# Kernel optimization log

Measured on AMD Instinct MI355X. Metric: run time of the kernel, lower is better.

## Reference

```python
import jax, jax.numpy as jnp
import numpy as np

NA = 50000   # nodes of type 'a'
NB = 50000   # nodes of type 'b'
E = 800000   # edges per cross relation
D = 256      # input feature dim == hidden_dim (SAGEConv lazy in-dim)
H = 256      # hidden_dim
EMB = 128    # embedding_dim
L = 2        # num_layer
# relation order in stacked weights: 0=(a,to,b), 1=(b,to,a), 2=(a,self_loop,a), 3=(b,self_loop,b)


def setup_inputs() -> dict:
    key = jax.random.key(0)
    ks = jax.random.split(key, 8)
    x_a = jax.random.normal(ks[0], (NA, D), jnp.float32)
    x_b = jax.random.normal(ks[1], (NB, D), jnp.float32)
    edge_ab = jax.random.randint(ks[2], (2, E), 0, NA, dtype=jnp.int32)  # row0: src in a, row1: dst in b
    edge_ba = jax.random.randint(ks[3], (2, E), 0, NB, dtype=jnp.int32)  # row0: src in b, row1: dst in a
    s = 1.0 / np.sqrt(H)
    Wl = jax.random.normal(ks[4], (L, 4, H, H), jnp.float32) * s  # lin_l weight (on aggregated neighbors)
    bl = jnp.zeros((L, 4, H), jnp.float32)                         # lin_l bias
    Wr = jax.random.normal(ks[5], (L, 4, H, H), jnp.float32) * s  # lin_r weight (root/self), no bias
    lin_W = jax.random.normal(ks[6], (H, EMB), jnp.float32) * s
    lin_b = jnp.zeros((EMB,), jnp.float32)
    return dict(x_a=x_a, x_b=x_b, edge_ab=edge_ab, edge_ba=edge_ba,
                Wl=Wl, bl=bl, Wr=Wr, lin_W=lin_W, lin_b=lin_b)


def _sage(x_src, x_dst, src, dst, n_dst, Wl, bl, Wr):
    # SAGEConv: mean-aggregate neighbor features, then lin_l(agg) + lin_r(x_dst)
    agg = jax.ops.segment_sum(x_src[src], dst, num_segments=n_dst)           # [n_dst, H]
    cnt = jax.ops.segment_sum(jnp.ones(src.shape, x_src.dtype), dst, num_segments=n_dst)
    mean = agg / jnp.maximum(cnt, 1.0)[:, None]                               # isolated dst -> 0
    return mean @ Wl + bl + x_dst @ Wr


def _sage_self(x, Wl, bl, Wr):
    # self-loop relation: each node has exactly one neighbor (itself), mean == x
    return x @ Wl + bl + x @ Wr


def reference(x_a, x_b, edge_ab, edge_ba, Wl, bl, Wr, lin_W, lin_b):
    xa, xb = x_a, x_b
    for l in range(L):
        new_a = (_sage(xb, xa, edge_ba[0], edge_ba[1], xa.shape[0], Wl[l, 1], bl[l, 1], Wr[l, 1])
                 + _sage_self(xa, Wl[l, 2], bl[l, 2], Wr[l, 2]))
        new_b = (_sage(xa, xb, edge_ab[0], edge_ab[1], xb.shape[0], Wl[l, 0], bl[l, 0], Wr[l, 0])
                 + _sage_self(xb, Wl[l, 3], bl[l, 3], Wr[l, 3]))
        xa, xb = jax.nn.relu(new_a), jax.nn.relu(new_b)
    return xa @ lin_W + lin_b, xb @ lin_W + lin_b
```

## Files before the change

kernel.cpp:

```cpp
#include <hip/hip_runtime.h>
#include <hip/hip_bf16.h>

#define NNA 50000
#define NNB 50000
#define NE  800000
#define HD  256
#define EMBD 128

typedef __attribute__((ext_vector_type(4))) int            i32x4;
typedef __attribute__((ext_vector_type(4))) float          f32x4;
typedef __attribute__((ext_vector_type(8))) short          bf16x8;
typedef __attribute__((ext_vector_type(4))) unsigned short u16x4;
typedef __attribute__((ext_vector_type(8))) unsigned short u16x8;

static __device__ __forceinline__ float bf2f(unsigned short u) {
  union { unsigned int i; float f; } v; v.i = ((unsigned int)u) << 16; return v.f;
}
static __device__ __forceinline__ unsigned short f2bf(float f) {
  __hip_bfloat16 h = __float2bfloat16(f);
  return *reinterpret_cast<unsigned short*>(&h);
}

static __device__ __forceinline__ void gload_lds16(const void* g, void* l) {
  __builtin_amdgcn_global_load_lds((const __attribute__((address_space(1))) void*)g,
                                   (__attribute__((address_space(3))) void*)l, 16, 0, 0);
}

__global__ void k_prep(const float* __restrict__ Wl, const float* __restrict__ Wr,
                       const float* __restrict__ bl, const float* __restrict__ linW,
                       unsigned short* __restrict__ WcatT, float* __restrict__ bias,
                       unsigned short* __restrict__ linWT) {
  int id = blockIdx.x * 256 + threadIdx.x;
  if (id < 2 * 2 * 512 * 256) {
    int n = id & 255;
    int k = (id >> 8) & 511;
    int t = (id >> 17) & 1;
    int l = id >> 18;
    int rn = (t == 0) ? 1 : 0;
    int rs = (t == 0) ? 2 : 3;
    float v;
    if (k < HD) {
      v = Wl[((l * 4 + rn) * HD + k) * HD + n];
    } else {
      int kk = k - HD;
      v = Wr[((l * 4 + rn) * HD + kk) * HD + n]
        + Wl[((l * 4 + rs) * HD + kk) * HD + n]
        + Wr[((l * 4 + rs) * HD + kk) * HD + n];
    }
    WcatT[((l * 2 + t) * HD + n) * 512 + k] = f2bf(v);
    return;
  }
  int id1 = id - 2 * 2 * 512 * 256;
  if (id1 < 2 * 2 * 256) {
    int n = id1 & 255; int t = (id1 >> 8) & 1; int l = id1 >> 9;
    int rn = (t == 0) ? 1 : 0;
    int rs = (t == 0) ? 2 : 3;
    bias[id1] = bl[(l * 4 + rn) * HD + n] + bl[(l * 4 + rs) * HD + n];
    return;
  }
  int id2 = id1 - 2 * 2 * 256;
  if (id2 < EMBD * HD) {
    int k = id2 & 255; int n = id2 >> 8;
    linWT[n * HD + k] = f2bf(linW[k * EMBD + n]);
  }
}

__global__ void k_convert(const float* __restrict__ xa, const float* __restrict__ xb,
                          unsigned short* __restrict__ out) {
  const int n4a = NNA * HD / 4;
  const int n4  = (NNA + NNB) * HD / 4;
  int i = blockIdx.x * blockDim.x + threadIdx.x;
  int stride = gridDim.x * blockDim.x;
  for (; i < n4; i += stride) {
    const float* src = (i < n4a) ? (xa + (size_t)i * 4) : (xb + (size_t)(i - n4a) * 4);
    f32x4 v = *reinterpret_cast<const f32x4*>(src);
    u16x4 o;
    o[0] = f2bf(v[0]); o[1] = f2bf(v[1]); o[2] = f2bf(v[2]); o[3] = f2bf(v[3]);
    reinterpret_cast<u16x4*>(out)[i] = o;
  }
}

__global__ void k_fill(const int* __restrict__ e_ba, const int* __restrict__ e_ab,
                       int* __restrict__ cnt_a, int* __restrict__ slots_a,
                       int* __restrict__ cnt_b, int* __restrict__ slots_b) {
  int e = blockIdx.x * 256 + threadIdx.x;
  if (e < NE) {
    int src = e_ba[e];
    int dst = e_ba[NE + e];
    int pos = atomicAdd(&cnt_a[dst], 1);
    if (pos < 64) slots_a[dst * 64 + pos] = src;
  } else if (e < 2 * NE) {
    int f = e - NE;
    int src = e_ab[f];
    int dst = e_ab[NE + f];
    int pos = atomicAdd(&cnt_b[dst], 1);
    if (pos < 64) slots_b[dst * 64 + pos] = src;
  }
}

__global__ __launch_bounds__(256)
void k_aggregate(const unsigned short* __restrict__ xa,
                 const unsigned short* __restrict__ xb,
                 const int* __restrict__ slots_a, const int* __restrict__ cnt_a,
                 const int* __restrict__ slots_b, const int* __restrict__ cnt_b,
                 unsigned short* __restrict__ mean_a, unsigned short* __restrict__ mean_b) {
  int w = blockIdx.x * 4 + (threadIdx.x >> 6);
  int lane = threadIdx.x & 63;
  const unsigned short* xsrc;
  const int* sl;
  int deg;
  unsigned short* outp;
  if (w < NNA) {
    xsrc = xb; sl = slots_a + (size_t)w * 64; deg = cnt_a[w];
    outp = mean_a + (size_t)w * HD;
  } else {
    int v = w - NNA;
    xsrc = xa; sl = slots_b + (size_t)v * 64; deg = cnt_b[v];
    outp = mean_b + (size_t)v * HD;
  }
  int m = deg < 64 ? deg : 64;
  int s_all = sl[lane];
  const int half = lane >> 5;
  const int l31 = lane & 31;

  float acc[8];
#pragma unroll
  for (int k = 0; k < 8; ++k) acc[k] = 0.f;

  int j = 0;
  for (; j + 8 <= m; j += 8) {
    int sj[4];
#pragma unroll
    for (int i = 0; i < 4; ++i) sj[i] = __shfl(s_all, j + 2 * i + half);
    u16x8 v[4];
#pragma unroll
    for (int i = 0; i < 4; ++i)
      v[i] = *reinterpret_cast<const u16x8*>(xsrc + (size_t)sj[i] * HD + l31 * 8);
#pragma unroll
    for (int i = 0; i < 4; ++i)
#pragma unroll
      for (int k = 0; k < 8; ++k) acc[k] += bf2f(v[i][k]);
  }
  for (; j + 2 <= m; j += 2) {
    int sj = __shfl(s_all, j + half);
    u16x8 v = *reinterpret_cast<const u16x8*>(xsrc + (size_t)sj * HD + l31 * 8);
#pragma unroll
    for (int k = 0; k < 8; ++k) acc[k] += bf2f(v[k]);
  }
  if (j < m && half == 0) {
    int sj = __shfl(s_all, j);
    u16x8 v = *reinterpret_cast<const u16x8*>(xsrc + (size_t)sj * HD + l31 * 8);
#pragma unroll
    for (int k = 0; k < 8; ++k) acc[k] += bf2f(v[k]);
  }

#pragma unroll
  for (int k = 0; k < 8; ++k) acc[k] += __shfl_xor(acc[k], 32);

  float inv = deg > 0 ? 1.0f / (float)deg : 0.0f;
  if (half == 0) {
    u16x8 o;
#pragma unroll
    for (int k = 0; k < 8; ++k) o[k] = f2bf(acc[k] * inv);
    *reinterpret_cast<u16x8*>(outp + l31 * 8) = o;
  }
}

template <bool RELU, bool OUTF32>
__global__ __launch_bounds__(256)
void k_gemm(const unsigned short* __restrict__ Alo,
            const unsigned short* __restrict__ Ahi,
            const unsigned short* __restrict__ BT,
            const float* __restrict__ bias,
            void* __restrict__ Cout,
            int M, int N, int Ktot, int Klo,
            long long sA, long long sB, long long sBias, long long sCbytes) {
  const int z = blockIdx.z;
  Alo += (long long)z * sA;
  Ahi += (long long)z * sA;
  BT += (long long)z * sB;
  bias += (long long)z * sBias;
  Cout = (void*)((char*)Cout + (long long)z * sCbytes);

  __shared__ char smem[65536];
  const int t = threadIdx.x;
  const int bm = blockIdx.x, bn = blockIdx.y;
  const int lane = t & 63, wid = t >> 6;
  const int wm = wid >> 1, wn = wid & 1;
  const int l15 = lane & 15, l4 = lane >> 4;
  const int rgrp = lane >> 3;
  const int boff = (((lane & 7) ^ rgrp) << 4);

  f32x4 acc[4][4];
#pragma unroll
  for (int i = 0; i < 4; ++i)
#pragma unroll
    for (int j = 0; j < 4; ++j) acc[i][j] = (f32x4){0.f, 0.f, 0.f, 0.f};

  const int nks = Ktot >> 6;

  auto stage = [&](int ks, int buf) {
    const int kglob = ks << 6;
    const unsigned short* Asrc = (kglob < Klo) ? Alo : Ahi;
    const int kbase = (kglob < Klo) ? kglob : (kglob - Klo);
    char* sA_ = smem + buf * 16384;
    char* sB_ = smem + 32768 + buf * 16384;
#pragma unroll
    for (int i = 0; i < 4; ++i) {
      int rloc = wid * 32 + i * 8;
      int rA = bm * 128 + rloc + rgrp;
      if (rA >= M) rA = M - 1;
      const char* ga = (const char*)(Asrc + (size_t)rA * HD + kbase) + boff;
      gload_lds16(ga, sA_ + rloc * 128);
      int rB = bn * 128 + rloc + rgrp;
      const char* gb = (const char*)(BT + (size_t)rB * Ktot + kglob) + boff;
      gload_lds16(gb, sB_ + rloc * 128);
    }
  };

  stage(0, 0);
  __syncthreads();

  for (int ks = 0; ks < nks; ++ks) {
    if (ks + 1 < nks) stage(ks + 1, (ks + 1) & 1);
    const char* sA_ = smem + (ks & 1) * 16384;
    const char* sB_ = smem + 32768 + (ks & 1) * 16384;
#pragma unroll
    for (int kk = 0; kk < 2; ++kk) {
      bf16x8 af[4], bfr[4];
#pragma unroll
      for (int f = 0; f < 4; ++f) {
        int r = wm * 64 + f * 16 + l15;
        af[f] = *reinterpret_cast<const bf16x8*>(
            sA_ + r * 128 + ((kk * 64 + l4 * 16) ^ ((r & 7) << 4)));
        int n = wn * 64 + f * 16 + l15;
        bfr[f] = *reinterpret_cast<const bf16x8*>(
            sB_ + n * 128 + ((kk * 64 + l4 * 16) ^ ((n & 7) << 4)));
      }
#pragma unroll
      for (int fm = 0; fm < 4; ++fm)
#pragma unroll
        for (int fn = 0; fn < 4; ++fn)
          acc[fm][fn] = __builtin_amdgcn_mfma_f32_16x16x32_bf16(af[fm], bfr[fn], acc[fm][fn], 0, 0, 0);
    }
    __syncthreads();
  }

#pragma unroll
  for (int fm = 0; fm < 4; ++fm) {
    int row0 = bm * 128 + wm * 64 + fm * 16 + l4 * 4;
#pragma unroll
    for (int fn = 0; fn < 4; ++fn) {
      int col = bn * 128 + wn * 64 + fn * 16 + l15;
      float bv = bias[col];
      f32x4 d = acc[fm][fn];
#pragma unroll
      for (int r = 0; r < 4; ++r) {
        int rg = row0 + r;
        if (rg < M) {
          float v = d[r] + bv;
          if (RELU) v = v > 0.f ? v : 0.f;
          if (OUTF32)
            reinterpret_cast<float*>(Cout)[(size_t)rg * N + col] = v;
          else
            reinterpret_cast<unsigned short*>(Cout)[(size_t)rg * N + col] = f2bf(v);
        }
      }
    }
  }
}


extern "C" void kernel_launch(void* const* d_in, const int* in_sizes, int n_in,
                              void* d_out, int out_size, void* d_ws, size_t ws_size,
                              hipStream_t stream) {
  const float* x_a  = (const float*)d_in[0];
  const float* x_b  = (const float*)d_in[1];
  const int*   e_ab = (const int*)d_in[2];
  const int*   e_ba = (const int*)d_in[3];
  const float* Wl   = (const float*)d_in[4];
  const float* bl   = (const float*)d_in[5];
  const float* Wr   = (const float*)d_in[6];
  const float* linW = (const float*)d_in[7];
  const float* linb = (const float*)d_in[8];
  float* out = (float*)d_out;

  char* ws = (char*)d_ws;
  size_t off = 0;
  auto alloc = [&](size_t bytes) {
    char* p = ws + off;
    off += (bytes + 255) & ~(size_t)255;
    return p;
  };
  unsigned short* x0   = (unsigned short*)alloc((size_t)2 * NNA * HD * 2);
  unsigned short* x1   = (unsigned short*)alloc((size_t)2 * NNA * HD * 2);
  unsigned short* mean = (unsigned short*)alloc((size_t)2 * NNA * HD * 2);
  int* slots_a = (int*)alloc((size_t)NNA * 64 * 4);
  int* slots_b = (int*)alloc((size_t)NNB * 64 * 4);
  int* cnt_a   = (int*)alloc((size_t)NNA * 4);
  int* cnt_b   = (int*)alloc((size_t)NNB * 4);
  unsigned short* wcatT  = (unsigned short*)alloc((size_t)2 * 2 * 256 * 512 * 2);
  float*          biasv  = (float*)alloc((size_t)2 * 2 * 256 * 4);
  unsigned short* linWT  = (unsigned short*)alloc((size_t)EMBD * HD * 2);
  (void)ws_size; (void)in_sizes; (void)n_in; (void)out_size;

  hipMemsetAsync(cnt_a, 0, (size_t)NNA * 4, stream);
  hipMemsetAsync(cnt_b, 0, (size_t)NNB * 4, stream);

  k_prep<<<(2 * 2 * 512 * 256 + 1024 + 32768 + 255) / 256, 256, 0, stream>>>(
      Wl, Wr, bl, linW, wcatT, biasv, linWT);
  k_convert<<<2048, 256, 0, stream>>>(x_a, x_b, x0);
  k_fill<<<(2 * NE + 255) / 256, 256, 0, stream>>>(e_ba, e_ab, cnt_a, slots_a, cnt_b, slots_b);

  unsigned short* xcur = x0;
  unsigned short* xnxt = x1;

  for (int l = 0; l < 2; ++l) {
    k_aggregate<<<(NNA + NNB) / 4, 256, 0, stream>>>(
        xcur, xcur + (size_t)NNA * HD, slots_a, cnt_a, slots_b, cnt_b,
        mean, mean + (size_t)NNA * HD);
    dim3 g((NNA + 127) / 128, 2, 2);
    k_gemm<true, false><<<g, 256, 0, stream>>>(
        mean, xcur, wcatT + (size_t)l * 2 * 256 * 512, biasv + l * 2 * 256, xnxt,
        NNA, 256, 512, 256,
        (long long)NNA * HD, 256 * 512, 256, (long long)NNA * HD * 2);
    unsigned short* tmp = xcur; xcur = xnxt; xnxt = tmp;
  }

  dim3 gf((NNA + 127) / 128, 1, 2);
  k_gemm<false, true><<<gf, 256, 0, stream>>>(
      xcur, xcur, linWT, linb, out,
      NNA, EMBD, 256, 256,
      (long long)NNA * HD, 0, 0, (long long)NNA * EMBD * 4);
}
```

Baseline: 527.5 us.

## Build compact CSR adjacency with 16-bit indices and fuse front-end kernels

```diff
diff --git a/kernel.cpp b/kernel.cpp
--- a/kernel.cpp
+++ b/kernel.cpp
@@ -7,6 +7,11 @@
 #define HD  256
 #define EMBD 128
 
+#define CONV_BLOCKS 2048
+#define COUNT_BLOCKS ((2 * NE) / 256)
+#define PREP_IDS (2 * 2 * 512 * 256 + 1024 + 32768)
+#define PREP_BLOCKS ((PREP_IDS + 255) / 256)
+
 typedef __attribute__((ext_vector_type(4))) int            i32x4;
 typedef __attribute__((ext_vector_type(4))) float          f32x4;
 typedef __attribute__((ext_vector_type(8))) short          bf16x8;
@@ -26,100 +31,143 @@
                                    (__attribute__((address_space(3))) void*)l, 16, 0, 0);
 }
 
-__global__ void k_prep(const float* __restrict__ Wl, const float* __restrict__ Wr,
-                       const float* __restrict__ bl, const float* __restrict__ linW,
-                       unsigned short* __restrict__ WcatT, float* __restrict__ bias,
-                       unsigned short* __restrict__ linWT) {
+__global__ __launch_bounds__(256)
+void k_front(const float* __restrict__ xa, const float* __restrict__ xb,
+             unsigned short* __restrict__ xout,
+             const int* __restrict__ e_ba, const int* __restrict__ e_ab,
+             int* __restrict__ cnt_a, int* __restrict__ cnt_b,
+             const float* __restrict__ Wl, const float* __restrict__ Wr,
+             const float* __restrict__ bl, const float* __restrict__ linW,
+             unsigned short* __restrict__ WcatT, float* __restrict__ bias,
+             unsigned short* __restrict__ linWT) {
+  int b = blockIdx.x;
+  if (b < CONV_BLOCKS) {
+    const int n4a = NNA * HD / 4;
+    const int n4  = (NNA + NNB) * HD / 4;
+    int i = b * 256 + threadIdx.x;
+    const int stride = CONV_BLOCKS * 256;
+    for (; i < n4; i += stride) {
+      const float* src = (i < n4a) ? (xa + (size_t)i * 4) : (xb + (size_t)(i - n4a) * 4);
+      f32x4 v = *reinterpret_cast<const f32x4*>(src);
+      u16x4 o;
+      o[0] = f2bf(v[0]); o[1] = f2bf(v[1]); o[2] = f2bf(v[2]); o[3] = f2bf(v[3]);
+      reinterpret_cast<u16x4*>(xout)[i] = o;
+    }
+    return;
+  }
+  b -= CONV_BLOCKS;
+  if (b < COUNT_BLOCKS) {
+    int e = b * 256 + threadIdx.x;
+    if (e < NE) {
+      int dst = e_ba[NE + e];
+      atomicAdd(&cnt_a[dst], 1);
+    } else {
+      int f = e - NE;
+      int dst = e_ab[NE + f];
+      atomicAdd(&cnt_b[dst], 1);
+    }
+    return;
+  }
+  b -= COUNT_BLOCKS;
+  {
+    int id = b * 256 + threadIdx.x;
+    if (id < 2 * 2 * 512 * 256) {
+      int n = id & 255;
+      int k = (id >> 8) & 511;
+      int t = (id >> 17) & 1;
+      int l = id >> 18;
+      int rn = (t == 0) ? 1 : 0;
+      int rs = (t == 0) ? 2 : 3;
+      float v;
+      if (k < HD) {
+        v = Wl[((l * 4 + rn) * HD + k) * HD + n];
+      } else {
+        int kk = k - HD;
+        v = Wr[((l * 4 + rn) * HD + kk) * HD + n]
+          + Wl[((l * 4 + rs) * HD + kk) * HD + n]
+          + Wr[((l * 4 + rs) * HD + kk) * HD + n];
+      }
+      WcatT[((l * 2 + t) * HD + n) * 512 + k] = f2bf(v);
+      return;
+    }
+    int id1 = id - 2 * 2 * 512 * 256;
+    if (id1 < 2 * 2 * 256) {
+      int n = id1 & 255; int t = (id1 >> 8) & 1; int l = id1 >> 9;
+      int rn = (t == 0) ? 1 : 0;
+      int rs = (t == 0) ? 2 : 3;
+      bias[id1] = bl[(l * 4 + rn) * HD + n] + bl[(l * 4 + rs) * HD + n];
+      return;
+    }
+    int id2 = id1 - 2 * 2 * 256;
+    if (id2 < EMBD * HD) {
+      int k = id2 & 255; int n = id2 >> 8;
+      linWT[n * HD + k] = f2bf(linW[k * EMBD + n]);
+    }
+  }
+}
+
+__global__ __launch_bounds__(256)
+void k_offsets(const int* __restrict__ cnt_a, const int* __restrict__ cnt_b,
+               unsigned* __restrict__ offs, unsigned* __restrict__ pos,
+               unsigned* __restrict__ tail) {
   int id = blockIdx.x * 256 + threadIdx.x;
-  if (id < 2 * 2 * 512 * 256) {
-    int n = id & 255;
-    int k = (id >> 8) & 511;
-    int t = (id >> 17) & 1;
-    int l = id >> 18;
-    int rn = (t == 0) ? 1 : 0;
-    int rs = (t == 0) ? 2 : 3;
-    float v;
-    if (k < HD) {
-      v = Wl[((l * 4 + rn) * HD + k) * HD + n];
-    } else {
-      int kk = k - HD;
-      v = Wr[((l * 4 + rn) * HD + kk) * HD + n]
-        + Wl[((l * 4 + rs) * HD + kk) * HD + n]
-        + Wr[((l * 4 + rs) * HD + kk) * HD + n];
-    }
-    WcatT[((l * 2 + t) * HD + n) * 512 + k] = f2bf(v);
-    return;
-  }
-  int id1 = id - 2 * 2 * 512 * 256;
-  if (id1 < 2 * 2 * 256) {
-    int n = id1 & 255; int t = (id1 >> 8) & 1; int l = id1 >> 9;
-    int rn = (t == 0) ? 1 : 0;
-    int rs = (t == 0) ? 2 : 3;
-    bias[id1] = bl[(l * 4 + rn) * HD + n] + bl[(l * 4 + rs) * HD + n];
-    return;
-  }
-  int id2 = id1 - 2 * 2 * 256;
-  if (id2 < EMBD * HD) {
-    int k = id2 & 255; int n = id2 >> 8;
-    linWT[n * HD + k] = f2bf(linW[k * EMBD + n]);
-  }
-}
-
-__global__ void k_convert(const float* __restrict__ xa, const float* __restrict__ xb,
-                          unsigned short* __restrict__ out) {
-  const int n4a = NNA * HD / 4;
-  const int n4  = (NNA + NNB) * HD / 4;
-  int i = blockIdx.x * blockDim.x + threadIdx.x;
-  int stride = gridDim.x * blockDim.x;
-  for (; i < n4; i += stride) {
-    const float* src = (i < n4a) ? (xa + (size_t)i * 4) : (xb + (size_t)(i - n4a) * 4);
-    f32x4 v = *reinterpret_cast<const f32x4*>(src);
-    u16x4 o;
-    o[0] = f2bf(v[0]); o[1] = f2bf(v[1]); o[2] = f2bf(v[2]); o[3] = f2bf(v[3]);
-    reinterpret_cast<u16x4*>(out)[i] = o;
-  }
-}
-
-__global__ void k_fill(const int* __restrict__ e_ba, const int* __restrict__ e_ab,
-                       int* __restrict__ cnt_a, int* __restrict__ slots_a,
-                       int* __restrict__ cnt_b, int* __restrict__ slots_b) {
+  int lane = threadIdx.x & 63;
+  unsigned deg = 0;
+  if (id < NNA) deg = (unsigned)cnt_a[id];
+  else if (id < NNA + NNB) deg = (unsigned)cnt_b[id - NNA];
+  unsigned v = deg;
+#pragma unroll
+  for (int d = 1; d < 64; d <<= 1) {
+    unsigned n = __shfl_up(v, d);
+    if (lane >= d) v += n;
+  }
+  unsigned tot = __shfl(v, 63);
+  unsigned base = 0;
+  if (lane == 0) base = atomicAdd(tail, tot);
+  base = __shfl(base, 0);
+  unsigned o = base + v - deg;
+  if (id < NNA + NNB) { offs[id] = o; pos[id] = o; }
+}
+
+__global__ __launch_bounds__(256)
+void k_scatter(const int* __restrict__ e_ba, const int* __restrict__ e_ab,
+               unsigned* __restrict__ pos, unsigned short* __restrict__ csr) {
   int e = blockIdx.x * 256 + threadIdx.x;
   if (e < NE) {
     int src = e_ba[e];
     int dst = e_ba[NE + e];
-    int pos = atomicAdd(&cnt_a[dst], 1);
-    if (pos < 64) slots_a[dst * 64 + pos] = src;
+    unsigned p = atomicAdd(&pos[dst], 1u);
+    csr[p] = (unsigned short)src;
   } else if (e < 2 * NE) {
     int f = e - NE;
     int src = e_ab[f];
     int dst = e_ab[NE + f];
-    int pos = atomicAdd(&cnt_b[dst], 1);
-    if (pos < 64) slots_b[dst * 64 + pos] = src;
+    unsigned p = atomicAdd(&pos[NNA + dst], 1u);
+    csr[p] = (unsigned short)src;
   }
 }
 
 __global__ __launch_bounds__(256)
 void k_aggregate(const unsigned short* __restrict__ xa,
                  const unsigned short* __restrict__ xb,
-                 const int* __restrict__ slots_a, const int* __restrict__ cnt_a,
-                 const int* __restrict__ slots_b, const int* __restrict__ cnt_b,
+                 const unsigned* __restrict__ offs,
+                 const int* __restrict__ cnt_a, const int* __restrict__ cnt_b,
+                 const unsigned short* __restrict__ csr,
                  unsigned short* __restrict__ mean_a, unsigned short* __restrict__ mean_b) {
   int w = blockIdx.x * 4 + (threadIdx.x >> 6);
   int lane = threadIdx.x & 63;
   const unsigned short* xsrc;
-  const int* sl;
   int deg;
   unsigned short* outp;
+  unsigned off0 = offs[w];
   if (w < NNA) {
-    xsrc = xb; sl = slots_a + (size_t)w * 64; deg = cnt_a[w];
+    xsrc = xb; deg = cnt_a[w];
     outp = mean_a + (size_t)w * HD;
   } else {
     int v = w - NNA;
-    xsrc = xa; sl = slots_b + (size_t)v * 64; deg = cnt_b[v];
+    xsrc = xa; deg = cnt_b[v];
     outp = mean_b + (size_t)v * HD;
   }
-  int m = deg < 64 ? deg : 64;
-  int s_all = sl[lane];
   const int half = lane >> 5;
   const int l31 = lane & 31;
 
@@ -127,31 +175,38 @@
 #pragma unroll
   for (int k = 0; k < 8; ++k) acc[k] = 0.f;
 
-  int j = 0;
-  for (; j + 8 <= m; j += 8) {
-    int sj[4];
-#pragma unroll
-    for (int i = 0; i < 4; ++i) sj[i] = __shfl(s_all, j + 2 * i + half);
-    u16x8 v[4];
-#pragma unroll
-    for (int i = 0; i < 4; ++i)
-      v[i] = *reinterpret_cast<const u16x8*>(xsrc + (size_t)sj[i] * HD + l31 * 8);
-#pragma unroll
-    for (int i = 0; i < 4; ++i)
-#pragma unroll
-      for (int k = 0; k < 8; ++k) acc[k] += bf2f(v[i][k]);
-  }
-  for (; j + 2 <= m; j += 2) {
-    int sj = __shfl(s_all, j + half);
-    u16x8 v = *reinterpret_cast<const u16x8*>(xsrc + (size_t)sj * HD + l31 * 8);
-#pragma unroll
-    for (int k = 0; k < 8; ++k) acc[k] += bf2f(v[k]);
-  }
-  if (j < m && half == 0) {
-    int sj = __shfl(s_all, j);
-    u16x8 v = *reinterpret_cast<const u16x8*>(xsrc + (size_t)sj * HD + l31 * 8);
-#pragma unroll
-    for (int k = 0; k < 8; ++k) acc[k] += bf2f(v[k]);
+  for (int j0 = 0; j0 < deg; j0 += 64) {
+    int mm = deg - j0;
+    if (mm > 64) mm = 64;
+    int s_all = 0;
+    if (j0 + lane < deg) s_all = (int)csr[off0 + j0 + lane];
+
+    int j = 0;
+    for (; j + 8 <= mm; j += 8) {
+      int sj[4];
+#pragma unroll
+      for (int i = 0; i < 4; ++i) sj[i] = __shfl(s_all, j + 2 * i + half);
+      u16x8 v[4];
+#pragma unroll
+      for (int i = 0; i < 4; ++i)
+        v[i] = *reinterpret_cast<const u16x8*>(xsrc + (size_t)sj[i] * HD + l31 * 8);
+#pragma unroll
+      for (int i = 0; i < 4; ++i)
+#pragma unroll
+        for (int k = 0; k < 8; ++k) acc[k] += bf2f(v[i][k]);
+    }
+    for (; j + 2 <= mm; j += 2) {
+      int sj = __shfl(s_all, j + half);
+      u16x8 v = *reinterpret_cast<const u16x8*>(xsrc + (size_t)sj * HD + l31 * 8);
+#pragma unroll
+      for (int k = 0; k < 8; ++k) acc[k] += bf2f(v[k]);
+    }
+    if (j < mm && half == 0) {
+      int sj = __shfl(s_all, j);
+      u16x8 v = *reinterpret_cast<const u16x8*>(xsrc + (size_t)sj * HD + l31 * 8);
+#pragma unroll
+      for (int k = 0; k < 8; ++k) acc[k] += bf2f(v[k]);
+    }
   }
 
 #pragma unroll
@@ -295,29 +350,30 @@
   unsigned short* x0   = (unsigned short*)alloc((size_t)2 * NNA * HD * 2);
   unsigned short* x1   = (unsigned short*)alloc((size_t)2 * NNA * HD * 2);
   unsigned short* mean = (unsigned short*)alloc((size_t)2 * NNA * HD * 2);
-  int* slots_a = (int*)alloc((size_t)NNA * 64 * 4);
-  int* slots_b = (int*)alloc((size_t)NNB * 64 * 4);
-  int* cnt_a   = (int*)alloc((size_t)NNA * 4);
-  int* cnt_b   = (int*)alloc((size_t)NNB * 4);
+  int*      cnt_a = (int*)alloc((size_t)(NNA + NNB + 64) * 4);
+  int*      cnt_b = cnt_a + NNA;
+  unsigned* tail  = (unsigned*)(cnt_a + NNA + NNB);
+  unsigned* offs  = (unsigned*)alloc((size_t)(NNA + NNB) * 4);
+  unsigned* pos   = (unsigned*)alloc((size_t)(NNA + NNB) * 4);
+  unsigned short* csr = (unsigned short*)alloc((size_t)(2 * NE + 64) * 2);
   unsigned short* wcatT  = (unsigned short*)alloc((size_t)2 * 2 * 256 * 512 * 2);
   float*          biasv  = (float*)alloc((size_t)2 * 2 * 256 * 4);
   unsigned short* linWT  = (unsigned short*)alloc((size_t)EMBD * HD * 2);
   (void)ws_size; (void)in_sizes; (void)n_in; (void)out_size;
 
-  hipMemsetAsync(cnt_a, 0, (size_t)NNA * 4, stream);
-  hipMemsetAsync(cnt_b, 0, (size_t)NNB * 4, stream);
-
-  k_prep<<<(2 * 2 * 512 * 256 + 1024 + 32768 + 255) / 256, 256, 0, stream>>>(
-      Wl, Wr, bl, linW, wcatT, biasv, linWT);
-  k_convert<<<2048, 256, 0, stream>>>(x_a, x_b, x0);
-  k_fill<<<(2 * NE + 255) / 256, 256, 0, stream>>>(e_ba, e_ab, cnt_a, slots_a, cnt_b, slots_b);
+  hipMemsetAsync(cnt_a, 0, (size_t)(NNA + NNB + 64) * 4, stream);
+
+  k_front<<<CONV_BLOCKS + COUNT_BLOCKS + PREP_BLOCKS, 256, 0, stream>>>(
+      x_a, x_b, x0, e_ba, e_ab, cnt_a, cnt_b, Wl, Wr, bl, linW, wcatT, biasv, linWT);
+  k_offsets<<<(NNA + NNB + 255) / 256, 256, 0, stream>>>(cnt_a, cnt_b, offs, pos, tail);
+  k_scatter<<<(2 * NE + 255) / 256, 256, 0, stream>>>(e_ba, e_ab, pos, csr);
 
   unsigned short* xcur = x0;
   unsigned short* xnxt = x1;
 
   for (int l = 0; l < 2; ++l) {
     k_aggregate<<<(NNA + NNB) / 4, 256, 0, stream>>>(
-        xcur, xcur + (size_t)NNA * HD, slots_a, cnt_a, slots_b, cnt_b,
+        xcur, xcur + (size_t)NNA * HD, offs, cnt_a, cnt_b, csr,
         mean, mean + (size_t)NNA * HD);
     dim3 g((NNA + 127) / 128, 2, 2);
     k_gemm<true, false><<<g, 256, 0, stream>>>(
```

After: 578.4 us. 9.6% more time.
